# Kernel tuning notes

Hardware: AMD Instinct MI355X
Metric: run time of the kernel (lower is better)

Reference implementation:

```python
import jax, jax.numpy as jnp
import numpy as np

T, B, V, E, HID, K = 1024, 128, 65536, 128, 256, 64
H = HID // 2  # per-direction LSTM hidden


def setup_inputs() -> dict:
    key = jax.random.key(0)
    ks = jax.random.split(key, 18)
    s = 0.05
    f32 = jnp.float32
    return {
        "kmers": jax.random.randint(ks[0], (T, B), 0, V),
        "tags": jax.random.randint(ks[1], (B,), 0, K),
        "emb": jax.random.normal(ks[2], (V, E), f32) * s,
        "w_ih_f": jax.random.normal(ks[3], (4 * H, E), f32) * s,
        "w_hh_f": jax.random.normal(ks[4], (4 * H, H), f32) * s,
        "b_ih_f": jax.random.normal(ks[5], (4 * H,), f32) * s,
        "b_hh_f": jax.random.normal(ks[6], (4 * H,), f32) * s,
        "w_ih_b": jax.random.normal(ks[7], (4 * H, E), f32) * s,
        "w_hh_b": jax.random.normal(ks[8], (4 * H, H), f32) * s,
        "b_ih_b": jax.random.normal(ks[9], (4 * H,), f32) * s,
        "b_hh_b": jax.random.normal(ks[10], (4 * H,), f32) * s,
        "w_proj": jax.random.normal(ks[11], (K, HID), f32) * s,
        "b_proj": jax.random.normal(ks[12], (K,), f32) * s,
        "start_trans": jax.random.uniform(ks[13], (K,), f32, -0.1, 0.1),
        "end_trans": jax.random.uniform(ks[14], (K,), f32, -0.1, 0.1),
        "trans": jax.random.uniform(ks[15], (K, K), f32, -0.1, 0.1),
    }


def _lstm_dir(x, w_ih, w_hh, b_ih, b_hh):
    # x: [T, B, E] -> hidden states [T, B, H]; PyTorch gate order i,f,g,o
    b = b_ih + b_hh
    xg = jnp.einsum('tbe,ge->tbg', x, w_ih) + b  # precompute input gates
    Bd = x.shape[1]
    Hd = w_hh.shape[1]
    def step(carry, g_in):
        h, c = carry
        g = g_in + h @ w_hh.T
        i, f, gg, o = jnp.split(g, 4, axis=-1)
        c = jax.nn.sigmoid(f) * c + jax.nn.sigmoid(i) * jnp.tanh(gg)
        h = jax.nn.sigmoid(o) * jnp.tanh(c)
        return (h, c), h
    init = (jnp.zeros((Bd, Hd), x.dtype), jnp.zeros((Bd, Hd), x.dtype))
    _, hs = jax.lax.scan(step, init, xg)
    return hs


def reference(kmers, tags, emb, w_ih_f, w_hh_f, b_ih_f, b_hh_f,
              w_ih_b, w_hh_b, b_ih_b, b_hh_b, w_proj, b_proj,
              start_trans, end_trans, trans):
    x = emb[kmers]  # [T, B, E]
    h_f = _lstm_dir(x, w_ih_f, w_hh_f, b_ih_f, b_hh_f)
    h_b = _lstm_dir(x[::-1], w_ih_b, w_hh_b, b_ih_b, b_hh_b)[::-1]
    out = jnp.concatenate([h_f, h_b], axis=-1)  # [T, B, HID]
    emissions = jnp.einsum('tbh,kh->tbk', out, w_proj) + b_proj  # [T, B, K]

    # tags repeated along time (original: tags.repeat(sent_size, 1))
    tags_seq = jnp.broadcast_to(tags[None, :], (emissions.shape[0], tags.shape[0]))

    # CRF numerator: score of given tag sequence (full mask)
    em_sel = jnp.take_along_axis(emissions, tags_seq[:, :, None], axis=2)[..., 0]  # [T, B]
    numerator = (start_trans[tags_seq[0]] + em_sel.sum(0)
                 + trans[tags_seq[:-1], tags_seq[1:]].sum(0)
                 + end_trans[tags_seq[-1]])  # [B]

    # CRF denominator: forward algorithm (log partition)
    def fwd_step(score, em_t):
        # score: [B, K] -> logsumexp over previous tag
        nxt = jax.nn.logsumexp(score[:, :, None] + trans[None, :, :] + em_t[:, None, :], axis=1)
        return nxt, None
    init = start_trans[None, :] + emissions[0]  # [B, K]
    final, _ = jax.lax.scan(fwd_step, init, emissions[1:])
    denominator = jax.nn.logsumexp(final + end_trans[None, :], axis=1)  # [B]

    # torchcrf default reduction='sum'; module returns negated llh
    return (denominator - numerator).sum()
```

## Files before the change

kernel.cpp:

```cpp
#include <hip/hip_runtime.h>
#include <hip/hip_bf16.h>

typedef _Float16 half8_t __attribute__((ext_vector_type(8)));
typedef _Float16 half4_t __attribute__((ext_vector_type(4)));
typedef _Float16 half2_t __attribute__((ext_vector_type(2)));
typedef float float4_t __attribute__((ext_vector_type(4)));
typedef unsigned int uint2_t __attribute__((ext_vector_type(2)));

#define TT 1024
#define BB 128
#define EE 128
#define HH 128
#define NTAG 64
#define ASTR 144

__device__ __forceinline__ float fast_exp(float x) {
  return __builtin_amdgcn_exp2f(x * 1.44269504088896f);
}
__device__ __forceinline__ void lds_barrier() {
  asm volatile("s_waitcnt lgkmcnt(0)\n\ts_barrier" ::: "memory");
}
__device__ __forceinline__ void lds_fence() {
  asm volatile("s_waitcnt lgkmcnt(0)" ::: "memory");
}
__device__ __forceinline__ half2_t cvt_pk(float a, float b) {
  return __builtin_bit_cast(half2_t, __builtin_amdgcn_cvt_pkrtz(a, b));
}
__device__ __forceinline__ half2_t h2bc(float v) {
  _Float16 h = (_Float16)v;
  half2_t r; r[0] = h; r[1] = h;
  return r;
}
__device__ __forceinline__ half8_t h8bc(float v) {
  _Float16 h = (_Float16)v;
  half8_t r;
#pragma unroll
  for (int i = 0; i < 8; ++i) r[i] = h;
  return r;
}
__device__ __forceinline__ float quad_max4(float v) {
  unsigned a = __builtin_bit_cast(unsigned, v);
  uint2_t r = __builtin_amdgcn_permlane32_swap(a, a, false, false);
  float m = fmaxf(__builtin_bit_cast(float, r[0]), __builtin_bit_cast(float, r[1]));
  unsigned b = __builtin_bit_cast(unsigned, m);
  uint2_t s = __builtin_amdgcn_permlane16_swap(b, b, false, false);
  return fmaxf(__builtin_bit_cast(float, s[0]), __builtin_bit_cast(float, s[1]));
}
__device__ __forceinline__ half2_t tanh6(half2_t x) {
  half2_t y = __builtin_elementwise_min(__builtin_elementwise_max(x, h2bc(-1.6f)), h2bc(1.6f));
  half2_t u = y * y;
  half2_t p = u * h2bc(0.04667f) + h2bc(-0.28507f);
  p = u * p + h2bc(1.0f);
  return y * p;
}
__device__ __forceinline__ half2_t sig6(half2_t x) {
  half2_t y = __builtin_elementwise_min(__builtin_elementwise_max(x, h2bc(-3.2f)), h2bc(3.2f));
  half2_t u = y * y;
  half2_t q = u * h2bc(0.00072921875f) + h2bc(-0.017816875f);
  q = u * q + h2bc(0.25f);
  return y * q + h2bc(0.5f);
}

__global__ __launch_bounds__(256) void init_kernel(float4_t* __restrict__ p) {
  p[blockIdx.x * 256 + threadIdx.x] = (float4_t){0.f, 0.f, 0.f, 0.f};
}

__global__ __launch_bounds__(256) void embed_kernel(const int* __restrict__ kmers,
                                                    const float* __restrict__ emb,
                                                    half4_t* __restrict__ x) {
  const int g = blockIdx.x * 256 + threadIdx.x;
  const int row = g >> 5, seg = g & 31;
  const int km = kmers[row];
  const float4_t v = ((const float4_t*)(emb + (size_t)km * EE))[seg];
  half4_t o;
  o[0] = (_Float16)v[0]; o[1] = (_Float16)v[1];
  o[2] = (_Float16)v[2]; o[3] = (_Float16)v[3];
  x[(size_t)row * 32 + seg] = o;
}

__device__ __forceinline__ void xg_body(
    int wg, const _Float16* __restrict__ x,
    const float* __restrict__ w_ih_f, const float* __restrict__ b_ih_f, const float* __restrict__ b_hh_f,
    const float* __restrict__ w_ih_b, const float* __restrict__ b_ih_b, const float* __restrict__ b_hh_b,
    _Float16* __restrict__ xgbuf, int s, int Tseg) {
  const int nt = Tseg >> 4;
  const int dir = wg / (8 * nt);
  const int rem = wg - dir * 8 * nt;
  const int chunk = rem / nt;
  const int tb = rem - chunk * nt;
  const int tid = threadIdx.x;
  const int wave = tid >> 6, lane = tid & 63;
  const int n16 = lane & 15, quad = lane >> 4;

  const float* wih = dir ? w_ih_b : w_ih_f;
  const float* bih = dir ? b_ih_b : b_ih_f;
  const float* bhh = dir ? b_hh_b : b_hh_f;

  half8_t wf[4][4];
#pragma unroll
  for (int g = 0; g < 4; ++g) {
    const int row = g * HH + wave * 16 + n16;
#pragma unroll
    for (int kf = 0; kf < 4; ++kf) {
      const float* src = wih + row * EE + kf * 32 + quad * 8;
#pragma unroll
      for (int i = 0; i < 8; ++i) wf[g][kf][i] = (_Float16)src[i];
    }
  }
  float4_t bias4[4];
#pragma unroll
  for (int g = 0; g < 4; ++g) {
    const int row = g * HH + wave * 16 + quad * 4;
    const float4_t bi = *(const float4_t*)(bih + row);
    const float4_t bh = *(const float4_t*)(bhh + row);
    bias4[g] = bi + bh;
  }

  const int l0 = tb * 16;
  half8_t xb[4];
  {
    const int te = dir ? (TT - 1 - (s * Tseg + l0)) : (s * Tseg + l0);
#pragma unroll
    for (int kf = 0; kf < 4; ++kf)
      xb[kf] = *(const half8_t*)(x + ((size_t)te * BB + chunk * 16 + n16) * EE + kf * 32 + quad * 8);
  }
  for (int u = 0; u < 16; ++u) {
    const int l = l0 + u;
    half8_t xn[4] = {};
    if (u < 15) {
      const int tn = dir ? (TT - 1 - (s * Tseg + l + 1)) : (s * Tseg + l + 1);
#pragma unroll
      for (int kf = 0; kf < 4; ++kf)
        xn[kf] = *(const half8_t*)(x + ((size_t)tn * BB + chunk * 16 + n16) * EE + kf * 32 + quad * 8);
    }
    float4_t acc[4];
#pragma unroll
    for (int g = 0; g < 4; ++g) acc[g] = bias4[g];
#pragma unroll
    for (int kf = 0; kf < 4; ++kf)
#pragma unroll
      for (int g = 0; g < 4; ++g)
        acc[g] = __builtin_amdgcn_mfma_f32_16x16x32_f16(wf[g][kf], xb[kf], acc[g], 0, 0, 0);
    half8_t ho0, ho1;
#pragma unroll
    for (int r = 0; r < 4; ++r) {
      ho0[r] = (_Float16)acc[0][r];
      ho0[4 + r] = (_Float16)acc[1][r];
      ho1[r] = (_Float16)acc[2][r];
      ho1[4 + r] = (_Float16)acc[3][r];
    }
    _Float16* ob = xgbuf + (size_t)dir * Tseg * 65536 + (size_t)l * 65536 + chunk * 8192 +
                   wave * 1024 + lane * 16;
    *(half8_t*)ob = ho0;
    *(half8_t*)(ob + 8) = ho1;
#pragma unroll
    for (int kf = 0; kf < 4; ++kf) xb[kf] = xn[kf];
  }
}

__global__ __launch_bounds__(512) void xg_kernel(
    const _Float16* __restrict__ x,
    const float* __restrict__ w_ih_f, const float* __restrict__ b_ih_f, const float* __restrict__ b_hh_f,
    const float* __restrict__ w_ih_b, const float* __restrict__ b_ih_b, const float* __restrict__ b_hh_b,
    _Float16* __restrict__ xgbuf, int s, int Tseg) {
  xg_body(blockIdx.x, x, w_ih_f, b_ih_f, b_hh_f, w_ih_b, b_ih_b, b_hh_b, xgbuf, s, Tseg);
}

__global__ __launch_bounds__(512, 2) void lstm_xg_kernel(
    const _Float16* __restrict__ xgrd, _Float16* __restrict__ xgwr,
    const _Float16* __restrict__ x,
    const float* __restrict__ w_hh_f, const float* __restrict__ w_hh_b,
    const float* __restrict__ w_ih_f, const float* __restrict__ b_ih_f, const float* __restrict__ b_hh_f,
    const float* __restrict__ w_ih_b, const float* __restrict__ b_ih_b, const float* __restrict__ b_hh_b,
    _Float16* __restrict__ h_cat, _Float16* __restrict__ h_state, float* __restrict__ c_state,
    int s, int sx, int Tseg) {
  __shared__ _Float16 A[2][16 * ASTR];
  if (blockIdx.x >= 16) {
    xg_body(blockIdx.x - 16, x, w_ih_f, b_ih_f, b_hh_f, w_ih_b, b_ih_b, b_hh_b, xgwr, sx, Tseg);
    return;
  }
  const int wg = blockIdx.x;
  const int dir = wg >> 3, chunk = wg & 7;
  const int b0 = chunk * 16;
  const float* w_hh = dir ? w_hh_b : w_hh_f;
  const int tid = threadIdx.x;
  const int wave = tid >> 6, lane = tid & 63;
  const int n16 = lane & 15, quad = lane >> 4;

  half8_t wf[4][4];
#pragma unroll
  for (int g = 0; g < 4; ++g) {
    const int row = g * HH + wave * 16 + n16;
#pragma unroll
    for (int kf = 0; kf < 4; ++kf) {
      const float* src = w_hh + row * HH + kf * 32 + quad * 8;
#pragma unroll
      for (int i = 0; i < 8; ++i) wf[g][kf][i] = (_Float16)src[i];
    }
  }
  const int sidx = ((wg * 8 + wave) * 64 + lane) * 4;
  half4_t h4 = *(const half4_t*)(h_state + sidx);
  float4_t c4 = *(const float4_t*)(c_state + sidx);
  half2_t c2[2];
  c2[0] = cvt_pk(c4[0], c4[1]);
  c2[1] = cvt_pk(c4[2], c4[3]);
  *(half4_t*)(&A[0][n16 * ASTR + wave * 16 + quad * 4]) = h4;

  const _Float16* xgw =
      xgrd + (size_t)dir * Tseg * 65536 + chunk * 8192 + wave * 1024 + (size_t)lane * 16;
  half4_t hlast = h4;
  const float4_t z4 = {0.f, 0.f, 0.f, 0.f};
  const int te0 = dir ? (TT - 1 - s * Tseg) : (s * Tseg);
  _Float16* gp_run =
      h_cat + ((size_t)te0 * BB + b0 + n16) * 256 + dir * HH + wave * 16 + quad * 4;
  const ptrdiff_t dstep = dir ? -(ptrdiff_t)32768 : (ptrdiff_t)32768;

  half8_t pf0[4], pf1[4];
#pragma unroll
  for (int j = 0; j < 4; ++j) {
    const _Float16* p = xgw + (size_t)j * 65536;
    pf0[j] = *(const half8_t*)p;
    pf1[j] = *(const half8_t*)(p + 8);
  }

#define LSTM_STEP(AB, AN, X0, X1)                                                          \
  {                                                                                        \
    const _Float16* Abp = &AB[0];                                                          \
    _Float16* Anp = &AN[0];                                                                \
    half8_t hb0 = *(const half8_t*)(Abp + n16 * ASTR + 0 * 32 + quad * 8);                 \
    half8_t hb1 = *(const half8_t*)(Abp + n16 * ASTR + 1 * 32 + quad * 8);                 \
    half8_t hb2 = *(const half8_t*)(Abp + n16 * ASTR + 2 * 32 + quad * 8);                 \
    half8_t hb3 = *(const half8_t*)(Abp + n16 * ASTR + 3 * 32 + quad * 8);                 \
    float4_t acc[4];                                                                       \
    _Pragma("unroll") for (int g = 0; g < 4; ++g) {                                        \
      acc[g] = __builtin_amdgcn_mfma_f32_16x16x32_f16(wf[g][0], hb0, z4, 0, 0, 0);         \
    }                                                                                      \
    _Pragma("unroll") for (int g = 0; g < 4; ++g) {                                        \
      acc[g] = __builtin_amdgcn_mfma_f32_16x16x32_f16(wf[g][1], hb1, acc[g], 0, 0, 0);     \
    }                                                                                      \
    _Pragma("unroll") for (int g = 0; g < 4; ++g) {                                        \
      acc[g] = __builtin_amdgcn_mfma_f32_16x16x32_f16(wf[g][2], hb2, acc[g], 0, 0, 0);     \
    }                                                                                      \
    _Pragma("unroll") for (int g = 0; g < 4; ++g) {                                        \
      acc[g] = __builtin_amdgcn_mfma_f32_16x16x32_f16(wf[g][3], hb3, acc[g], 0, 0, 0);     \
    }                                                                                      \
    const half2_t* x0p = (const half2_t*)&X0;                                              \
    const half2_t* x1p = (const half2_t*)&X1;                                              \
    half4_t hstore;                                                                        \
    _Pragma("unroll") for (int p = 0; p < 2; ++p) {                                        \
      const half2_t i_ = sig6(cvt_pk(acc[0][2 * p], acc[0][2 * p + 1]) + x0p[p]);          \
      const half2_t f_ = sig6(cvt_pk(acc[1][2 * p], acc[1][2 * p + 1]) + x0p[2 + p]);      \
      const half2_t g_ = tanh6(cvt_pk(acc[2][2 * p], acc[2][2 * p + 1]) + x1p[p]);         \
      const half2_t o_ = sig6(cvt_pk(acc[3][2 * p], acc[3][2 * p + 1]) + x1p[2 + p]);      \
      c2[p] = f_ * c2[p] + i_ * g_;                                                        \
      const half2_t hh = o_ * tanh6(c2[p]);                                                \
      hstore[2 * p] = hh[0];                                                               \
      hstore[2 * p + 1] = hh[1];                                                           \
    }                                                                                      \
    *(half4_t*)(Anp + n16 * ASTR + wave * 16 + quad * 4) = hstore;                         \
    *(half4_t*)gp_run = hstore;                                                            \
    hlast = hstore;                                                                        \
  }

  for (int il = 0; il < Tseg - 4; il += 4) {
#pragma unroll
    for (int j = 0; j < 4; ++j) {
      lds_barrier();
      if (j & 1) {
        LSTM_STEP(A[1], A[0], pf0[j], pf1[j]);
      } else {
        LSTM_STEP(A[0], A[1], pf0[j], pf1[j]);
      }
      const _Float16* p = xgw + (size_t)(il + j + 4) * 65536;
      pf0[j] = *(const half8_t*)p;
      pf1[j] = *(const half8_t*)(p + 8);
      gp_run += dstep;
    }
  }
#pragma unroll
  for (int j = 0; j < 4; ++j) {
    lds_barrier();
    if (j & 1) {
      LSTM_STEP(A[1], A[0], pf0[j], pf1[j]);
    } else {
      LSTM_STEP(A[0], A[1], pf0[j], pf1[j]);
    }
    gp_run += dstep;
  }
#undef LSTM_STEP

  *(half4_t*)(h_state + sidx) = hlast;
  c4[0] = (float)c2[0][0]; c4[1] = (float)c2[0][1];
  c4[2] = (float)c2[1][0]; c4[3] = (float)c2[1][1];
  *(float4_t*)(c_state + sidx) = c4;
}

__global__ __launch_bounds__(256) void emis_kernel(const _Float16* __restrict__ h_cat,
                                                   const float* __restrict__ w_proj,
                                                   const float* __restrict__ b_proj,
                                                   float* __restrict__ em,
                                                   _Float16* __restrict__ expem) {
  const int tid = threadIdx.x;
  const int wave = tid >> 6, lane = tid & 63;
  const int n16 = lane & 15, quad = lane >> 4;
  const size_t row0 = (size_t)blockIdx.x * 64 + wave * 16;

  half8_t bf[4][8];
#pragma unroll
  for (int nt = 0; nt < 4; ++nt) {
    const float* wp = w_proj + (nt * 16 + n16) * 256;
#pragma unroll
    for (int kf = 0; kf < 8; ++kf) {
      const int kb = kf * 32 + quad * 8;
#pragma unroll
      for (int i = 0; i < 8; ++i) bf[nt][kf][i] = (_Float16)wp[kb + i];
    }
  }
  float4_t acc[4];
#pragma unroll
  for (int nt = 0; nt < 4; ++nt) {
    const float bv = b_proj[nt * 16 + n16];
    acc[nt] = (float4_t){bv, bv, bv, bv};
  }
#pragma unroll
  for (int kf = 0; kf < 8; ++kf) {
    half8_t af = *(const half8_t*)(h_cat + (row0 + n16) * 256 + kf * 32 + quad * 8);
#pragma unroll
    for (int nt = 0; nt < 4; ++nt)
      acc[nt] = __builtin_amdgcn_mfma_f32_16x16x32_f16(af, bf[nt][kf], acc[nt], 0, 0, 0);
  }
#pragma unroll
  for (int nt = 0; nt < 4; ++nt)
#pragma unroll
    for (int r = 0; r < 4; ++r) {
      const size_t idx = (row0 + quad * 4 + r) * NTAG + nt * 16 + n16;
      em[idx] = acc[nt][r];
      expem[idx] = (_Float16)fast_exp(acc[nt][r]);
    }
}

__global__ __launch_bounds__(64) void mcrf_kernel(const float* __restrict__ em,
                                                  const _Float16* __restrict__ expem,
                                                  const float* __restrict__ trans,
                                                  const int* __restrict__ tags,
                                                  const float* __restrict__ start_trans,
                                                  const float* __restrict__ end_trans,
                                                  _Float16* __restrict__ Nbuf,
                                                  float* __restrict__ lzbuf,
                                                  float* __restrict__ num) {
  const int lane = threadIdx.x;
  if (blockIdx.x >= 2048) {
    const int nb = blockIdx.x - 2048;
    const int tg = tags[nb];
    float acc = 0.f;
    for (int t = lane; t < TT; t += 64)
      acc += em[((size_t)t * BB + nb) * NTAG + tg];
#pragma unroll
    for (int off = 32; off > 0; off >>= 1) acc += __shfl_xor(acc, off, 64);
    if (lane == 0)
      num[nb] = start_trans[tg] + end_trans[tg] + 1023.0f * trans[tg * NTAG + tg] + acc;
    return;
  }
  const int n16 = lane & 15, quad = lane >> 4;
  const int b = blockIdx.x >> 4;
  const int s = blockIdx.x & 15;

  half8_t efA[4][2];
#pragma unroll
  for (int mt = 0; mt < 4; ++mt)
#pragma unroll
    for (int kf = 0; kf < 2; ++kf)
#pragma unroll
      for (int i = 0; i < 8; ++i) {
        const int m = mt * 16 + n16, k = kf * 32 + quad * 8 + i;
        efA[mt][kf][i] = (_Float16)(fast_exp(trans[k * NTAG + m]) * 0.015625f);
      }

  half8_t pb[4][2];
#pragma unroll
  for (int tile = 0; tile < 4; ++tile)
#pragma unroll
    for (int kf = 0; kf < 2; ++kf)
#pragma unroll
      for (int i = 0; i < 8; ++i) {
        const int k = kf * 32 + quad * 8 + i;
        pb[tile][kf][i] = (_Float16)((k == tile * 16 + n16) ? 1.f : 0.f);
      }

  float lz2 = 0.f;
  const float4_t z4 = {0.f, 0.f, 0.f, 0.f};
  const _Float16* exb = expem + (size_t)b * NTAG;
  const int t0 = s * 64 + 1;
  const int nsteps = (s == 15) ? 63 : 64;

#define MCRF_CORE(PB0, PB1, NB0, NB1)                                                      \
  {                                                                                        \
    float4_t a0 = __builtin_amdgcn_mfma_f32_16x16x32_f16(efA[0][0], PB0, z4, 0, 0, 0);     \
    float4_t a1 = __builtin_amdgcn_mfma_f32_16x16x32_f16(efA[1][0], PB0, z4, 0, 0, 0);     \
    float4_t a2 = __builtin_amdgcn_mfma_f32_16x16x32_f16(efA[2][0], PB0, z4, 0, 0, 0);     \
    float4_t a3 = __builtin_amdgcn_mfma_f32_16x16x32_f16(efA[3][0], PB0, z4, 0, 0, 0);     \
    a0 = __builtin_amdgcn_mfma_f32_16x16x32_f16(efA[0][1], PB1, a0, 0, 0, 0);              \
    a1 = __builtin_amdgcn_mfma_f32_16x16x32_f16(efA[1][1], PB1, a1, 0, 0, 0);              \
    a2 = __builtin_amdgcn_mfma_f32_16x16x32_f16(efA[2][1], PB1, a2, 0, 0, 0);              \
    a3 = __builtin_amdgcn_mfma_f32_16x16x32_f16(efA[3][1], PB1, a3, 0, 0, 0);              \
    half2_t dpk[4][2];                                                                     \
    dpk[0][0] = cvt_pk(a0[0], a0[1]); dpk[0][1] = cvt_pk(a0[2], a0[3]);                    \
    dpk[1][0] = cvt_pk(a1[0], a1[1]); dpk[1][1] = cvt_pk(a1[2], a1[3]);                    \
    dpk[2][0] = cvt_pk(a2[0], a2[1]); dpk[2][1] = cvt_pk(a2[2], a2[3]);                    \
    dpk[3][0] = cvt_pk(a3[0], a3[1]); dpk[3][1] = cvt_pk(a3[2], a3[3]);                    \
    half2_t* wwp0 = (half2_t*)&NB0;                                                        \
    half2_t* wwp1 = (half2_t*)&NB1;                                                        \
    _Pragma("unroll") for (int kf = 0; kf < 2; ++kf) {                                     \
      half2_t* wp = kf ? wwp1 : wwp0;                                                      \
      _Pragma("unroll") for (int p = 0; p < 2; ++p) {                                      \
        const unsigned Xu = __builtin_bit_cast(unsigned, dpk[2 * kf][p]);                  \
        const unsigned Yu = __builtin_bit_cast(unsigned, dpk[2 * kf + 1][p]);              \
        uint2_t r1 = __builtin_amdgcn_permlane32_swap(Xu, Yu, false, false);               \
        uint2_t r2 = __builtin_amdgcn_permlane16_swap(r1[0], r1[1], false, false);         \
        wp[p] = __builtin_bit_cast(half2_t, r2[0]);                                        \
        wp[2 + p] = __builtin_bit_cast(half2_t, r2[1]);                                    \
      }                                                                                    \
    }                                                                                      \
  }

#define MSTEP(GC0, GC1, IT)                                                                \
  {                                                                                        \
    _Pragma("unroll") for (int tile = 0; tile < 4; ++tile) {                               \
      half8_t nb0, nb1;                                                                    \
      MCRF_CORE(pb[tile][0], pb[tile][1], nb0, nb1)                                        \
      pb[tile][0] = nb0 * GC0;                                                             \
      pb[tile][1] = nb1 * GC1;                                                             \
    }                                                                                      \
    if (((IT) & 15) == 15) {                                                               \
      half8_t m8 = __builtin_elementwise_max(pb[0][0], pb[0][1]);                          \
      m8 = __builtin_elementwise_max(m8, __builtin_elementwise_max(pb[1][0], pb[1][1]));   \
      m8 = __builtin_elementwise_max(m8, __builtin_elementwise_max(pb[2][0], pb[2][1]));   \
      m8 = __builtin_elementwise_max(m8, __builtin_elementwise_max(pb[3][0], pb[3][1]));   \
      float mm = (float)m8[0];                                                             \
      _Pragma("unroll") for (int i = 1; i < 8; ++i) mm = fmaxf(mm, (float)m8[i]);          \
      mm = quad_max4(mm);                                                                  \
      mm = fmaxf(mm, __shfl_xor(mm, 1, 64));                                               \
      mm = fmaxf(mm, __shfl_xor(mm, 2, 64));                                               \
      mm = fmaxf(mm, __shfl_xor(mm, 4, 64));                                               \
      mm = fmaxf(mm, __shfl_xor(mm, 8, 64));                                               \
      lz2 += __builtin_amdgcn_logf(mm);                                                    \
      const half8_t rc8 = h8bc(__builtin_amdgcn_rcpf(mm));                                 \
      _Pragma("unroll") for (int tile = 0; tile < 4; ++tile) {                             \
        pb[tile][0] *= rc8;                                                                \
        pb[tile][1] *= rc8;                                                                \
      }                                                                                    \
    }                                                                                      \
  }

  half8_t pre0[4], pre1[4];
#pragma unroll
  for (int j = 0; j < 4; ++j) {
    const size_t tt = (size_t)(t0 + j) * 8192;
    pre0[j] = *(const half8_t*)(exb + tt + quad * 8);
    pre1[j] = *(const half8_t*)(exb + tt + 32 + quad * 8);
  }
  int it = 0;
  const int full4 = nsteps >> 2;
  for (int grp = 0; grp < full4; ++grp) {
#pragma unroll
    for (int j = 0; j < 4; ++j) {
      const half8_t gc0 = pre0[j], gc1 = pre1[j];
      int tf = t0 + it + 4;
      tf = tf > 1023 ? 1023 : tf;
      const size_t tt = (size_t)tf * 8192;
      pre0[j] = *(const half8_t*)(exb + tt + quad * 8);
      pre1[j] = *(const half8_t*)(exb + tt + 32 + quad * 8);
      MSTEP(gc0, gc1, it)
      ++it;
    }
  }
  for (; it < nsteps; ++it) {
    const size_t tt = (size_t)(t0 + it) * 8192;
    const half8_t gc0 = *(const half8_t*)(exb + tt + quad * 8);
    const half8_t gc1 = *(const half8_t*)(exb + tt + 32 + quad * 8);
    MSTEP(gc0, gc1, it)
  }
#undef MSTEP
#undef MCRF_CORE

  _Float16* nb = Nbuf + ((size_t)b * 16 + s) * 4096;
#pragma unroll
  for (int tile = 0; tile < 4; ++tile) {
    const int col = tile * 16 + n16;
#pragma unroll
    for (int kf = 0; kf < 2; ++kf)
      *(half8_t*)(nb + (size_t)col * 64 + kf * 32 + quad * 8) = pb[tile][kf];
  }
  if (lane == 0) lzbuf[b * 16 + s] = lz2;
}

__global__ __launch_bounds__(64) void merge_kernel(const _Float16* __restrict__ Nbuf,
                                                   const float* __restrict__ lzbuf,
                                                   const float* __restrict__ em,
                                                   const float* __restrict__ start_trans,
                                                   const float* __restrict__ end_trans,
                                                   float* __restrict__ denom) {
  const int b = blockIdx.x, m = threadIdx.x;
  __shared__ float w[64];
  float L2 = 0.f;
  w[m] = fast_exp(end_trans[m]);
  for (int s = 15; s >= 0; --s) {
    lds_fence();
    const _Float16* row = Nbuf + (((size_t)b * 16 + s) * 64 + m) * 64;
    float acc = 0.f;
#pragma unroll
    for (int kf = 0; kf < 8; ++kf) {
      const half8_t rv = *(const half8_t*)(row + kf * 8);
#pragma unroll
      for (int i = 0; i < 8; ++i) acc += (float)rv[i] * w[kf * 8 + i];
    }
    float mx = acc;
#pragma unroll
    for (int off = 32; off > 0; off >>= 1) mx = fmaxf(mx, __shfl_xor(mx, off, 64));
    L2 += __builtin_amdgcn_logf(mx) + lzbuf[b * 16 + s];
    const float inv = __builtin_amdgcn_rcpf(mx);
    lds_fence();
    w[m] = acc * inv;
  }
  lds_fence();
  const float sv = start_trans[m] + em[(size_t)b * NTAG + m];
  float m0 = sv;
#pragma unroll
  for (int off = 32; off > 0; off >>= 1) m0 = fmaxf(m0, __shfl_xor(m0, off, 64));
  float z = fast_exp(sv - m0) * w[m];
#pragma unroll
  for (int off = 32; off > 0; off >>= 1) z += __shfl_xor(z, off, 64);
  if (m == 0)
    denom[b] = m0 + 0.693147180559945f * (L2 + 6138.0f + __builtin_amdgcn_logf(z));
}

__global__ __launch_bounds__(128) void final_kernel(const float* __restrict__ denom,
                                                    const float* __restrict__ num,
                                                    float* __restrict__ out) {
  const int tid = threadIdx.x;
  float v = denom[tid] - num[tid];
#pragma unroll
  for (int off = 32; off > 0; off >>= 1) v += __shfl_xor(v, off, 64);
  __shared__ float red[2];
  if ((tid & 63) == 0) red[tid >> 6] = v;
  __syncthreads();
  if (tid == 0) out[0] = red[0] + red[1];
}

extern "C" void kernel_launch(void* const* d_in, const int* in_sizes, int n_in,
                              void* d_out, int out_size, void* d_ws, size_t ws_size,
                              hipStream_t stream) {
  const int* kmers = (const int*)d_in[0];
  const int* tags = (const int*)d_in[1];
  const float* emb = (const float*)d_in[2];
  const float* w_ih_f = (const float*)d_in[3];
  const float* w_hh_f = (const float*)d_in[4];
  const float* b_ih_f = (const float*)d_in[5];
  const float* b_hh_f = (const float*)d_in[6];
  const float* w_ih_b = (const float*)d_in[7];
  const float* w_hh_b = (const float*)d_in[8];
  const float* b_ih_b = (const float*)d_in[9];
  const float* b_hh_b = (const float*)d_in[10];
  const float* w_proj = (const float*)d_in[11];
  const float* b_proj = (const float*)d_in[12];
  const float* start_trans = (const float*)d_in[13];
  const float* end_trans = (const float*)d_in[14];
  const float* trans = (const float*)d_in[15];

  char* ws = (char*)d_ws;
  half4_t* x = (half4_t*)ws;
  _Float16* h_cat = (_Float16*)(ws + 33554432);
  float* em = (float*)ws;
  float* out = (float*)d_out;
  _Float16* Nbuf = (_Float16*)(ws + 33554432);
  float* lzbuf = (float*)(ws + 33554432 + 16777216);
  float* denom = (float*)(ws + 33554432 + 16785408);
  float* num = (float*)(ws + 33554432 + 16785920);

  const bool fused = ws_size >= 235078656ull;
  if (fused) {
    const int Tseg = 256;
    _Float16* buf0 = (_Float16*)(ws + 100663296);
    _Float16* buf1 = (_Float16*)(ws + 100663296 + 67108864);
    _Float16* expem = (_Float16*)(ws + 100663296);
    _Float16* h_state = (_Float16*)(ws + 100663296 + 134217728);
    float* c_state = (float*)(ws + 100663296 + 134217728 + 65536);

    hipLaunchKernelGGL(init_kernel, dim3(48), dim3(256), 0, stream, (float4_t*)h_state);
    hipLaunchKernelGGL(embed_kernel, dim3(16384), dim3(256), 0, stream, kmers, emb, x);
    hipLaunchKernelGGL(xg_kernel, dim3(Tseg), dim3(512), 0, stream, (const _Float16*)x,
                       w_ih_f, b_ih_f, b_hh_f, w_ih_b, b_ih_b, b_hh_b, buf0, 0, Tseg);
    for (int s = 0; s < 3; ++s) {
      _Float16* rd = (s & 1) ? buf1 : buf0;
      _Float16* wr = (s & 1) ? buf0 : buf1;
      hipLaunchKernelGGL(lstm_xg_kernel, dim3(16 + Tseg), dim3(512), 0, stream,
                         (const _Float16*)rd, wr, (const _Float16*)x, w_hh_f, w_hh_b,
                         w_ih_f, b_ih_f, b_hh_f, w_ih_b, b_ih_b, b_hh_b,
                         h_cat, h_state, c_state, s, s + 1, Tseg);
    }
    hipLaunchKernelGGL(lstm_xg_kernel, dim3(16), dim3(512), 0, stream,
                       (const _Float16*)buf1, buf0, (const _Float16*)x, w_hh_f, w_hh_b,
                       w_ih_f, b_ih_f, b_hh_f, w_ih_b, b_ih_b, b_hh_b,
                       h_cat, h_state, c_state, 3, 0, Tseg);
    hipLaunchKernelGGL(emis_kernel, dim3(2048), dim3(256), 0, stream, h_cat, w_proj, b_proj, em,
                       expem);
    hipLaunchKernelGGL(mcrf_kernel, dim3(2176), dim3(64), 0, stream, em,
                       (const _Float16*)expem, trans, tags, start_trans, end_trans, Nbuf, lzbuf,
                       num);
    hipLaunchKernelGGL(merge_kernel, dim3(128), dim3(64), 0, stream, (const _Float16*)Nbuf,
                       lzbuf, em, start_trans, end_trans, denom);
    hipLaunchKernelGGL(final_kernel, dim3(1), dim3(128), 0, stream, denom, num, out);
  } else {
    int nseg;
    if (ws_size >= 167969792ull) nseg = 4;
    else if (ws_size >= 134415360ull) nseg = 8;
    else nseg = 16;
    const int Tseg = TT / nseg;
    const size_t xg_bytes = 268435456ull / (size_t)nseg;
    _Float16* xgbuf = (_Float16*)(ws + 100663296);
    _Float16* expem = (_Float16*)(ws + 100663296);
    _Float16* h_state = (_Float16*)(ws + 100663296 + xg_bytes);
    float* c_state = (float*)(ws + 100663296 + xg_bytes + 65536);

    hipLaunchKernelGGL(init_kernel, dim3(48), dim3(256), 0, stream, (float4_t*)h_state);
    hipLaunchKernelGGL(embed_kernel, dim3(16384), dim3(256), 0, stream, kmers, emb, x);
    for (int s = 0; s < nseg; ++s) {
      hipLaunchKernelGGL(xg_kernel, dim3(Tseg), dim3(512), 0, stream, (const _Float16*)x,
                         w_ih_f, b_ih_f, b_hh_f, w_ih_b, b_ih_b, b_hh_b, xgbuf, s, Tseg);
      hipLaunchKernelGGL(lstm_xg_kernel, dim3(16), dim3(512), 0, stream,
                         (const _Float16*)xgbuf, xgbuf, (const _Float16*)x, w_hh_f, w_hh_b,
                         w_ih_f, b_ih_f, b_hh_f, w_ih_b, b_ih_b, b_hh_b,
                         h_cat, h_state, c_state, s, s, Tseg);
    }
    hipLaunchKernelGGL(emis_kernel, dim3(2048), dim3(256), 0, stream, h_cat, w_proj, b_proj, em,
                       expem);
    hipLaunchKernelGGL(mcrf_kernel, dim3(2176), dim3(64), 0, stream, em,
                       (const _Float16*)expem, trans, tags, start_trans, end_trans, Nbuf, lzbuf,
                       num);
    hipLaunchKernelGGL(merge_kernel, dim3(128), dim3(64), 0, stream, (const _Float16*)Nbuf,
                       lzbuf, em, start_trans, end_trans, denom);
    hipLaunchKernelGGL(final_kernel, dim3(1), dim3(128), 0, stream, denom, num, out);
  }
}
```

Before: 959.7 us.

## Pack both LSTM directions into 1024-thread blocks and fuse init with embed

The recurrent LSTM kernel now runs both directions for a batch chunk inside one 1024-thread workgroup, with separate LDS double buffers per direction. The overlapped xg work is packed two units per block, and a large unused shared-memory pad limits residency so recurrent blocks get a CU to themselves. The zero-init and embedding kernels are merged into one launch to save a kernel dispatch. The change puts two independent recurrences under one shared barrier, so each wave waits on the other direction's waves as well, and the pad reduces co-residency for the xg blocks.

New measurement: 3.158 ms. 3.29x slower.

```diff
diff --git a/kernel.cpp b/kernel.cpp
--- a/kernel.cpp
+++ b/kernel.cpp
@@ -61,14 +61,15 @@
   return y * q + h2bc(0.5f);
 }
 
-__global__ __launch_bounds__(256) void init_kernel(float4_t* __restrict__ p) {
-  p[blockIdx.x * 256 + threadIdx.x] = (float4_t){0.f, 0.f, 0.f, 0.f};
-}
-
-__global__ __launch_bounds__(256) void embed_kernel(const int* __restrict__ kmers,
-                                                    const float* __restrict__ emb,
-                                                    half4_t* __restrict__ x) {
-  const int g = blockIdx.x * 256 + threadIdx.x;
+__global__ __launch_bounds__(256) void initembed_kernel(const int* __restrict__ kmers,
+                                                        const float* __restrict__ emb,
+                                                        half4_t* __restrict__ x,
+                                                        float4_t* __restrict__ state) {
+  if (blockIdx.x < 48) {
+    state[blockIdx.x * 256 + threadIdx.x] = (float4_t){0.f, 0.f, 0.f, 0.f};
+    return;
+  }
+  const int g = (blockIdx.x - 48) * 256 + threadIdx.x;
   const int row = g >> 5, seg = g & 31;
   const int km = kmers[row];
   const float4_t v = ((const float4_t*)(emb + (size_t)km * EE))[seg];
@@ -79,7 +80,7 @@
 }
 
 __device__ __forceinline__ void xg_body(
-    int wg, const _Float16* __restrict__ x,
+    int wg, int tid, const _Float16* __restrict__ x,
     const float* __restrict__ w_ih_f, const float* __restrict__ b_ih_f, const float* __restrict__ b_hh_f,
     const float* __restrict__ w_ih_b, const float* __restrict__ b_ih_b, const float* __restrict__ b_hh_b,
     _Float16* __restrict__ xgbuf, int s, int Tseg) {
@@ -88,7 +89,6 @@
   const int rem = wg - dir * 8 * nt;
   const int chunk = rem / nt;
   const int tb = rem - chunk * nt;
-  const int tid = threadIdx.x;
   const int wave = tid >> 6, lane = tid & 63;
   const int n16 = lane & 15, quad = lane >> 4;
 
@@ -163,10 +163,11 @@
     const float* __restrict__ w_ih_f, const float* __restrict__ b_ih_f, const float* __restrict__ b_hh_f,
     const float* __restrict__ w_ih_b, const float* __restrict__ b_ih_b, const float* __restrict__ b_hh_b,
     _Float16* __restrict__ xgbuf, int s, int Tseg) {
-  xg_body(blockIdx.x, x, w_ih_f, b_ih_f, b_hh_f, w_ih_b, b_ih_b, b_hh_b, xgbuf, s, Tseg);
-}
-
-__global__ __launch_bounds__(512, 2) void lstm_xg_kernel(
+  xg_body(blockIdx.x, threadIdx.x, x, w_ih_f, b_ih_f, b_hh_f, w_ih_b, b_ih_b, b_hh_b, xgbuf, s,
+          Tseg);
+}
+
+__global__ __launch_bounds__(1024) void lstm_xg_kernel(
     const _Float16* __restrict__ xgrd, _Float16* __restrict__ xgwr,
     const _Float16* __restrict__ x,
     const float* __restrict__ w_hh_f, const float* __restrict__ w_hh_b,
@@ -174,23 +175,28 @@
     const float* __restrict__ w_ih_b, const float* __restrict__ b_ih_b, const float* __restrict__ b_hh_b,
     _Float16* __restrict__ h_cat, _Float16* __restrict__ h_state, float* __restrict__ c_state,
     int s, int sx, int Tseg) {
-  __shared__ _Float16 A[2][16 * ASTR];
-  if (blockIdx.x >= 16) {
-    xg_body(blockIdx.x - 16, x, w_ih_f, b_ih_f, b_hh_f, w_ih_b, b_ih_b, b_hh_b, xgwr, sx, Tseg);
+  __shared__ _Float16 A[2][2][16 * ASTR];
+  __shared__ char occupancy_pad[81920];
+  if (s == -123456) occupancy_pad[threadIdx.x] = 1;
+
+  if (blockIdx.x >= 8) {
+    const int unit = (blockIdx.x - 8) * 2 + (threadIdx.x >> 9);
+    xg_body(unit, threadIdx.x & 511, x, w_ih_f, b_ih_f, b_hh_f, w_ih_b, b_ih_b, b_hh_b, xgwr,
+            sx, Tseg);
     return;
   }
-  const int wg = blockIdx.x;
-  const int dir = wg >> 3, chunk = wg & 7;
+  const int chunk = blockIdx.x;
   const int b0 = chunk * 16;
+  const int tid = threadIdx.x;
+  const int wave16 = tid >> 6, lane = tid & 63;
+  const int dir = wave16 >> 3, w = wave16 & 7;
+  const int n16 = lane & 15, quad = lane >> 4;
   const float* w_hh = dir ? w_hh_b : w_hh_f;
-  const int tid = threadIdx.x;
-  const int wave = tid >> 6, lane = tid & 63;
-  const int n16 = lane & 15, quad = lane >> 4;
 
   half8_t wf[4][4];
 #pragma unroll
   for (int g = 0; g < 4; ++g) {
-    const int row = g * HH + wave * 16 + n16;
+    const int row = g * HH + w * 16 + n16;
 #pragma unroll
     for (int kf = 0; kf < 4; ++kf) {
       const float* src = w_hh + row * HH + kf * 32 + quad * 8;
@@ -198,21 +204,20 @@
       for (int i = 0; i < 8; ++i) wf[g][kf][i] = (_Float16)src[i];
     }
   }
-  const int sidx = ((wg * 8 + wave) * 64 + lane) * 4;
+  const int sidx = (((dir * 8 + chunk) * 8 + w) * 64 + lane) * 4;
   half4_t h4 = *(const half4_t*)(h_state + sidx);
   float4_t c4 = *(const float4_t*)(c_state + sidx);
   half2_t c2[2];
   c2[0] = cvt_pk(c4[0], c4[1]);
   c2[1] = cvt_pk(c4[2], c4[3]);
-  *(half4_t*)(&A[0][n16 * ASTR + wave * 16 + quad * 4]) = h4;
+  *(half4_t*)(&A[dir][0][n16 * ASTR + w * 16 + quad * 4]) = h4;
 
   const _Float16* xgw =
-      xgrd + (size_t)dir * Tseg * 65536 + chunk * 8192 + wave * 1024 + (size_t)lane * 16;
+      xgrd + (size_t)dir * Tseg * 65536 + chunk * 8192 + w * 1024 + (size_t)lane * 16;
   half4_t hlast = h4;
   const float4_t z4 = {0.f, 0.f, 0.f, 0.f};
   const int te0 = dir ? (TT - 1 - s * Tseg) : (s * Tseg);
-  _Float16* gp_run =
-      h_cat + ((size_t)te0 * BB + b0 + n16) * 256 + dir * HH + wave * 16 + quad * 4;
+  _Float16* gp_run = h_cat + ((size_t)te0 * BB + b0 + n16) * 256 + dir * HH + w * 16 + quad * 4;
   const ptrdiff_t dstep = dir ? -(ptrdiff_t)32768 : (ptrdiff_t)32768;
 
   half8_t pf0[4], pf1[4];
@@ -222,11 +227,13 @@
     pf0[j] = *(const half8_t*)p;
     pf1[j] = *(const half8_t*)(p + 8);
   }
+  _Float16* const Ad0 = &A[dir][0][0];
+  _Float16* const Ad1 = &A[dir][1][0];
 
 #define LSTM_STEP(AB, AN, X0, X1)                                                          \
   {                                                                                        \
-    const _Float16* Abp = &AB[0];                                                          \
-    _Float16* Anp = &AN[0];                                                                \
+    const _Float16* Abp = AB;                                                              \
+    _Float16* Anp = AN;                                                                    \
     half8_t hb0 = *(const half8_t*)(Abp + n16 * ASTR + 0 * 32 + quad * 8);                 \
     half8_t hb1 = *(const half8_t*)(Abp + n16 * ASTR + 1 * 32 + quad * 8);                 \
     half8_t hb2 = *(const half8_t*)(Abp + n16 * ASTR + 2 * 32 + quad * 8);                 \
@@ -257,7 +264,7 @@
       hstore[2 * p] = hh[0];                                                               \
       hstore[2 * p + 1] = hh[1];                                                           \
     }                                                                                      \
-    *(half4_t*)(Anp + n16 * ASTR + wave * 16 + quad * 4) = hstore;                         \
+    *(half4_t*)(Anp + n16 * ASTR + w * 16 + quad * 4) = hstore;                            \
     *(half4_t*)gp_run = hstore;                                                            \
     hlast = hstore;                                                                        \
   }
@@ -267,9 +274,9 @@
     for (int j = 0; j < 4; ++j) {
       lds_barrier();
       if (j & 1) {
-        LSTM_STEP(A[1], A[0], pf0[j], pf1[j]);
+        LSTM_STEP(Ad1, Ad0, pf0[j], pf1[j]);
       } else {
-        LSTM_STEP(A[0], A[1], pf0[j], pf1[j]);
+        LSTM_STEP(Ad0, Ad1, pf0[j], pf1[j]);
       }
       const _Float16* p = xgw + (size_t)(il + j + 4) * 65536;
       pf0[j] = *(const half8_t*)p;
@@ -281,9 +288,9 @@
   for (int j = 0; j < 4; ++j) {
     lds_barrier();
     if (j & 1) {
-      LSTM_STEP(A[1], A[0], pf0[j], pf1[j]);
+      LSTM_STEP(Ad1, Ad0, pf0[j], pf1[j]);
     } else {
-      LSTM_STEP(A[0], A[1], pf0[j], pf1[j]);
+      LSTM_STEP(Ad0, Ad1, pf0[j], pf1[j]);
     }
     gp_run += dstep;
   }
@@ -586,19 +593,19 @@
     _Float16* h_state = (_Float16*)(ws + 100663296 + 134217728);
     float* c_state = (float*)(ws + 100663296 + 134217728 + 65536);
 
-    hipLaunchKernelGGL(init_kernel, dim3(48), dim3(256), 0, stream, (float4_t*)h_state);
-    hipLaunchKernelGGL(embed_kernel, dim3(16384), dim3(256), 0, stream, kmers, emb, x);
+    hipLaunchKernelGGL(initembed_kernel, dim3(16432), dim3(256), 0, stream, kmers, emb, x,
+                       (float4_t*)h_state);
     hipLaunchKernelGGL(xg_kernel, dim3(Tseg), dim3(512), 0, stream, (const _Float16*)x,
                        w_ih_f, b_ih_f, b_hh_f, w_ih_b, b_ih_b, b_hh_b, buf0, 0, Tseg);
     for (int s = 0; s < 3; ++s) {
       _Float16* rd = (s & 1) ? buf1 : buf0;
       _Float16* wr = (s & 1) ? buf0 : buf1;
-      hipLaunchKernelGGL(lstm_xg_kernel, dim3(16 + Tseg), dim3(512), 0, stream,
+      hipLaunchKernelGGL(lstm_xg_kernel, dim3(8 + Tseg / 2), dim3(1024), 0, stream,
                          (const _Float16*)rd, wr, (const _Float16*)x, w_hh_f, w_hh_b,
                          w_ih_f, b_ih_f, b_hh_f, w_ih_b, b_ih_b, b_hh_b,
                          h_cat, h_state, c_state, s, s + 1, Tseg);
     }
-    hipLaunchKernelGGL(lstm_xg_kernel, dim3(16), dim3(512), 0, stream,
+    hipLaunchKernelGGL(lstm_xg_kernel, dim3(8), dim3(1024), 0, stream,
                        (const _Float16*)buf1, buf0, (const _Float16*)x, w_hh_f, w_hh_b,
                        w_ih_f, b_ih_f, b_hh_f, w_ih_b, b_ih_b, b_hh_b,
                        h_cat, h_state, c_state, 3, 0, Tseg);
@@ -622,12 +629,12 @@
     _Float16* h_state = (_Float16*)(ws + 100663296 + xg_bytes);
     float* c_state = (float*)(ws + 100663296 + xg_bytes + 65536);
 
-    hipLaunchKernelGGL(init_kernel, dim3(48), dim3(256), 0, stream, (float4_t*)h_state);
-    hipLaunchKernelGGL(embed_kernel, dim3(16384), dim3(256), 0, stream, kmers, emb, x);
+    hipLaunchKernelGGL(initembed_kernel, dim3(16432), dim3(256), 0, stream, kmers, emb, x,
+                       (float4_t*)h_state);
     for (int s = 0; s < nseg; ++s) {
       hipLaunchKernelGGL(xg_kernel, dim3(Tseg), dim3(512), 0, stream, (const _Float16*)x,
                          w_ih_f, b_ih_f, b_hh_f, w_ih_b, b_ih_b, b_hh_b, xgbuf, s, Tseg);
-      hipLaunchKernelGGL(lstm_xg_kernel, dim3(16), dim3(512), 0, stream,
+      hipLaunchKernelGGL(lstm_xg_kernel, dim3(8), dim3(1024), 0, stream,
                          (const _Float16*)xgbuf, xgbuf, (const _Float16*)x, w_hh_f, w_hh_b,
                          w_ih_f, b_ih_f, b_hh_f, w_ih_b, b_ih_b, b_hh_b,
                          h_cat, h_state, c_state, s, s, Tseg);
```
